# Kernel tuning notes

Hardware: AMD Instinct MI355X
Metric: run time of the kernel (lower is better)

## Reference

```python
import jax, jax.numpy as jnp
import numpy as np

G = 4        # number of grids (batch)
L = 16384    # voxels per grid (equal-length grids)
P = 512      # patch_size
H = 8        # num_heads


def setup_inputs() -> dict:
    key = jax.random.key(0)
    k1, k2, k3, k4, k5, k6 = jax.random.split(key, 6)
    N, C = G * L, 512
    feats = jax.random.normal(k1, (N, C), dtype=jnp.float32)
    curve_codes = jax.random.randint(k2, (N,), 0, 1 << 30, dtype=jnp.int64)
    Wqkv = jax.random.normal(k3, (3 * C, C), dtype=jnp.float32) * 0.02
    bqkv = jax.random.normal(k4, (3 * C,), dtype=jnp.float32) * 0.02
    Wproj = jax.random.normal(k5, (C, C), dtype=jnp.float32) * 0.02
    bproj = jax.random.normal(k6, (C,), dtype=jnp.float32) * 0.02
    return {"feats": feats, "curve_codes": curve_codes, "Wqkv": Wqkv,
            "bqkv": bqkv, "Wproj": Wproj, "bproj": bproj}


def reference(feats, curve_codes, Wqkv, bqkv, Wproj, bproj):
    N, C = feats.shape
    D = C // H
    scale = D ** -0.5
    # per-grid space-filling-curve sort -> global permutation indices
    codes = curve_codes.reshape(G, L)
    perm = (jnp.argsort(codes, axis=1) + jnp.arange(G)[:, None] * L).reshape(N)
    x = feats[perm]                                   # curve-sorted voxels
    qkv = x @ Wqkv.T + bqkv                           # [N, 3C]
    # contiguous patches of size P (grid lengths divisible by P)
    qkv = qkv.reshape(N // P, P, 3, H, D)
    q, k, v = qkv[:, :, 0], qkv[:, :, 1], qkv[:, :, 2]  # [nP, P, H, D]
    scores = jnp.einsum('nphd,nqhd->nhpq', q, k) * scale
    attn = jax.nn.softmax(scores, axis=-1)
    out = jnp.einsum('nhpq,nqhd->nphd', attn, v).reshape(N, C)
    # inverse permutation: out_final[perm[j]] = out[j]
    out = jnp.zeros_like(out).at[perm].set(out)
    return out @ Wproj.T + bproj
```

## Files before the change

kernel.cpp:

```cpp
#include <hip/hip_runtime.h>
#include <hip/hip_bf16.h>


typedef unsigned long long u64;
typedef unsigned short ushort_t;
typedef __attribute__((ext_vector_type(8))) short short8v;
typedef __attribute__((ext_vector_type(4))) float f32x4;

#define MFMA_BF16 __builtin_amdgcn_mfma_f32_16x16x32_bf16

__device__ __forceinline__ unsigned short f2bf(float f) {
  union { float f; unsigned u; } v; v.f = f;
  return (unsigned short)((v.u + 0x7FFFu + ((v.u >> 16) & 1u)) >> 16);
}

__device__ __forceinline__ unsigned pk2(float a, float b) {
  __hip_bfloat162 h = __float22bfloat162_rn(float2{a, b});
  unsigned u; __builtin_memcpy(&u, &h, 4); return u;
}

__device__ __forceinline__ void async16(ushort_t* lds, const ushort_t* g) {
  __builtin_amdgcn_global_load_lds(
      (const __attribute__((address_space(1))) unsigned int*)g,
      (__attribute__((address_space(3))) unsigned int*)lds, 16, 0, 0);
}


__global__ __launch_bounds__(512) void sort_chunk(const int* __restrict__ codes,
                                                  u64* __restrict__ keys) {
  __shared__ u64 sk[4096];
  const int base = blockIdx.x * 4096;
  for (int t = threadIdx.x; t < 4096; t += 512) {
    int e = base + t;
    sk[t] = (((u64)(unsigned)codes[e]) << 14) | (u64)(e & 16383);
  }
  __syncthreads();
  for (int k = 2; k <= 4096; k <<= 1) {
    for (int j = k >> 1; j > 0; j >>= 1) {
      for (int t = threadIdx.x; t < 4096; t += 512) {
        int jx = t ^ j;
        if (jx > t) {
          bool up = (((base + t) & 16383 & k) == 0);
          u64 a = sk[t], b = sk[jx];
          if ((a > b) == up) { sk[t] = b; sk[jx] = a; }
        }
      }
      __syncthreads();
    }
  }
  for (int t = threadIdx.x; t < 4096; t += 512) keys[base + t] = sk[t];
}

__global__ __launch_bounds__(256) void sort_gpass(u64* __restrict__ keys, int k, int j) {
  int t = blockIdx.x * 256 + threadIdx.x;
  int jx = t ^ j;
  if (jx > t) {
    bool up = ((t & 16383 & k) == 0);
    u64 a = keys[t], b = keys[jx];
    if ((a > b) == up) { keys[t] = b; keys[jx] = a; }
  }
}

__global__ __launch_bounds__(512) void sort_finish(u64* __restrict__ keys, int k) {
  __shared__ u64 sk[4096];
  const int base = blockIdx.x * 4096;
  for (int t = threadIdx.x; t < 4096; t += 512) sk[t] = keys[base + t];
  __syncthreads();
  for (int j = 2048; j > 0; j >>= 1) {
    for (int t = threadIdx.x; t < 4096; t += 512) {
      int jx = t ^ j;
      if (jx > t) {
        bool up = (((base + t) & 16383 & k) == 0);
        u64 a = sk[t], b = sk[jx];
        if ((a > b) == up) { sk[t] = b; sk[jx] = a; }
      }
    }
    __syncthreads();
  }
  for (int t = threadIdx.x; t < 4096; t += 512) keys[base + t] = sk[t];
}

__global__ __launch_bounds__(256) void write_perm(const u64* __restrict__ keys,
                                                  int* __restrict__ perm) {
  int t = blockIdx.x * 256 + threadIdx.x;
  int g = t >> 14;
  int a = (int)(keys[t] & 16383);
  perm[t] = (g << 14) | a;
}


__global__ __launch_bounds__(256) void gather_bf16(const float* __restrict__ feats,
    const int* __restrict__ perm, ushort_t* __restrict__ A) {
  int t = blockIdx.x * 256 + threadIdx.x;
  int m = t >> 5;
  int off = (t & 31) << 4;
  const float* src = feats + (size_t)perm[m] * 512 + off;
  float4 a = ((const float4*)src)[0];
  float4 b = ((const float4*)src)[1];
  float4 c = ((const float4*)src)[2];
  float4 d = ((const float4*)src)[3];
  short8v lo = { (short)f2bf(a.x), (short)f2bf(a.y), (short)f2bf(a.z), (short)f2bf(a.w),
                 (short)f2bf(b.x), (short)f2bf(b.y), (short)f2bf(b.z), (short)f2bf(b.w) };
  short8v hi = { (short)f2bf(c.x), (short)f2bf(c.y), (short)f2bf(c.z), (short)f2bf(c.w),
                 (short)f2bf(d.x), (short)f2bf(d.y), (short)f2bf(d.z), (short)f2bf(d.w) };
  ushort_t* dst = A + (size_t)m * 512 + off;
  *(short8v*)(dst) = lo;
  *(short8v*)(dst + 8) = hi;
}

__global__ __launch_bounds__(256) void convert_bf16(const float* __restrict__ src,
                                                    ushort_t* __restrict__ dst) {
  int t = blockIdx.x * 256 + threadIdx.x;
  const float* s = src + (size_t)t * 8;
  float4 a = ((const float4*)s)[0];
  float4 b = ((const float4*)s)[1];
  short8v v = { (short)f2bf(a.x), (short)f2bf(a.y), (short)f2bf(a.z), (short)f2bf(a.w),
                (short)f2bf(b.x), (short)f2bf(b.y), (short)f2bf(b.z), (short)f2bf(b.w) };
  *(short8v*)(dst + (size_t)t * 8) = v;
}


__global__ __launch_bounds__(256) void qkv_gemm(const ushort_t* __restrict__ A,
    const ushort_t* __restrict__ W, const float* __restrict__ bias,
    ushort_t* __restrict__ Q, ushort_t* __restrict__ Ko, ushort_t* __restrict__ Vt)
{
  __shared__ __align__(16) ushort_t la[128 * 64];
  __shared__ __align__(16) ushort_t lb[128 * 64];
  const int bid = blockIdx.x;
  const int swz = (bid & 7) * 768 + (bid >> 3);
  const int bx = swz % 12, by = swz / 12;
  const int rowBase = by * 128, colBase = bx * 128;
  const int tid = threadIdx.x, lane = tid & 63, w = tid >> 6;
  const int wr = w >> 1, wc = w & 1;
  const int li = lane & 15, kb = lane >> 4;
  const int lr = lane >> 3;
  const int lcs = (((lane & 7) ^ lr) << 3);
  f32x4 acc[4][4] = {};
  for (int kt = 0; kt < 8; ++kt) {
#pragma unroll
    for (int i = 0; i < 4; ++i) {
      int c = w * 4 + i;
      async16(la + c * 512, A + (size_t)(rowBase + c * 8 + lr) * 512 + kt * 64 + lcs);
      async16(lb + c * 512, W + (size_t)(colBase + c * 8 + lr) * 512 + kt * 64 + lcs);
    }
    __syncthreads();
    short8v af[2][4], bfr[2][4];
#pragma unroll
    for (int kk = 0; kk < 2; ++kk)
#pragma unroll
      for (int t = 0; t < 4; ++t) {
        int sl = ((kk * 4 + kb) ^ (li & 7)) << 3;
        af[kk][t]  = *(const short8v*)(la + (wr * 64 + t * 16 + li) * 64 + sl);
        bfr[kk][t] = *(const short8v*)(lb + (wc * 64 + t * 16 + li) * 64 + sl);
      }
#pragma unroll
    for (int kk = 0; kk < 2; ++kk)
#pragma unroll
      for (int i = 0; i < 4; ++i)
#pragma unroll
        for (int j = 0; j < 4; ++j)
          acc[i][j] = MFMA_BF16(af[kk][i], bfr[kk][j], acc[i][j], 0, 0, 0);
    __syncthreads();
  }
  const int c0 = colBase + wc * 64;
  ushort_t* tw = (w < 2) ? (la + w * 4096) : (lb + (w - 2) * 4096);
  if (c0 >= 1024) {
    char* twb = (char*)tw;
#pragma unroll
    for (int j = 0; j < 4; ++j) {
      int dloc = j * 16 + li;
      float bv = bias[c0 + dloc];
#pragma unroll
      for (int i = 0; i < 4; ++i) {
        unsigned u0 = pk2(acc[i][j][0] + bv, acc[i][j][1] + bv);
        unsigned u1 = pk2(acc[i][j][2] + bv, acc[i][j][3] + bv);
        int s = i * 2 + (kb >> 1);
        int byte = dloc * 128 + ((s ^ (dloc & 7)) << 4) + ((kb & 1) << 3);
        *(uint2*)(twb + byte) = make_uint2(u0, u1);
      }
    }
    const int h = (c0 - 1024) >> 6;
    const size_t nh = (size_t)((rowBase >> 9) * 8 + h);
    const int pbase = ((rowBase + wr * 64) & 511) + ((lane & 7) << 3);
    ushort_t* vb = Vt + nh * 32768 + pbase;
#pragma unroll
    for (int ps = 0; ps < 8; ++ps) {
      int dloc = ps * 8 + (lane >> 3);
      int byte = dloc * 128 + ((((lane & 7)) ^ (dloc & 7)) << 4);
      short8v vv = *(const short8v*)(twb + byte);
      *(short8v*)(vb + dloc * 512) = vv;
    }
  } else {
    const bool isQ = (c0 >> 9) == 0;
    const float qs = isQ ? 0.180336879f : 1.0f;
    unsigned* twd = (unsigned*)tw;
#pragma unroll
    for (int j = 0; j < 4; ++j) {
      int dl = j * 16 + li;
      float bv = bias[c0 + dl];
#pragma unroll
      for (int i = 0; i < 4; ++i)
#pragma unroll
        for (int r = 0; r < 4; ++r) {
          int p = i * 16 + kb * 4 + r;
          unsigned short hv = f2bf((acc[i][j][r] + bv) * qs);
          int dw = (dl >> 1) ^ (kb << 3);
          *((ushort_t*)(twd + p * 32 + dw) + (dl & 1)) = hv;
        }
    }
    const int hq = (c0 >> 6) & 7;
    const size_t nh = (size_t)((rowBase >> 9) * 8 + hq);
    const int p0w = (rowBase + wr * 64) & 511;
    ushort_t* qb = (isQ ? Q : Ko) + (nh * 512 + p0w) * 64 + ((lane & 7) << 3);
    const int prow = lane >> 3;
#pragma unroll
    for (int ps = 0; ps < 8; ++ps) {
      int p = ps * 8 + prow;
      int dw0 = ((lane & 7) << 2) ^ ((((p >> 2) & 3)) << 3);
      short8v vv = *(const short8v*)(twd + p * 32 + dw0);
      *(short8v*)(qb + (size_t)p * 64) = vv;
    }
  }
}


#define TILE_EXP(S, LACC, PB) do {                                             \
  _Pragma("unroll")                                                            \
  for (int t = 0; t < 4; ++t)                                                  \
    _Pragma("unroll")                                                          \
    for (int r = 0; r < 4; ++r) S[t][r] = exp2f(S[t][r]);                      \
  float q0 = (S[0][0] + S[0][1]) + (S[0][2] + S[0][3]);                        \
  float q1 = (S[1][0] + S[1][1]) + (S[1][2] + S[1][3]);                        \
  float q2 = (S[2][0] + S[2][1]) + (S[2][2] + S[2][3]);                        \
  float q3 = (S[3][0] + S[3][1]) + (S[3][2] + S[3][3]);                        \
  LACC += (q0 + q1) + (q2 + q3);                                               \
  _Pragma("unroll")                                                            \
  for (int t = 0; t < 4; ++t) {                                                \
    unsigned plo = pk2(S[t][0], S[t][1]);                                      \
    unsigned phi = pk2(S[t][2], S[t][3]);                                      \
    *(uint2*)((char*)(PB) + (((2 * t + (kb >> 1)) << 8) | (li << 4) |          \
                             ((kb & 1) << 3))) = make_uint2(plo, phi);         \
  }                                                                            \
} while (0)

__global__ __launch_bounds__(256, 2) void attn_kernel(const ushort_t* __restrict__ Q,
    const ushort_t* __restrict__ K, const ushort_t* __restrict__ Vt,
    const int* __restrict__ perm, ushort_t* __restrict__ O)
{
  __shared__ __align__(16) ushort_t kbuf[2][64][64];
  __shared__ __align__(16) ushort_t vbuf[2][64][64];
  __shared__ __align__(16) ushort_t pbuf[4][1024];
  const int b = blockIdx.x;
  const int qc = (b >> 3) & 3;
  const int nh = ((b >> 5) << 3) | (b & 7);
  const int n = nh >> 3, h = nh & 7;
  const int tid = threadIdx.x, w = tid >> 6, lane = tid & 63;
  const int li = lane & 15, kb = lane >> 4;
  const ushort_t* Qb = Q + (size_t)nh * (512 * 64);
  const ushort_t* Kb = K + (size_t)nh * (512 * 64);
  const ushort_t* Vb = Vt + (size_t)nh * (64 * 512);
  const int p0 = qc * 128 + w * 32;

  const int srow = lane >> 3;
  const int ssw = (((lane & 7) ^ srow) << 3);
  const ushort_t* Ksrc = Kb + (size_t)(w * 8 + srow) * 64 + ssw;
  const ushort_t* Vsrc = Vb + (size_t)(w * 8 + srow) * 512 + ssw;

  short8v qa0 = *(const short8v*)(Qb + (size_t)(p0 + li) * 64 + kb * 8);
  short8v qa1 = *(const short8v*)(Qb + (size_t)(p0 + li) * 64 + 32 + kb * 8);
  short8v qb0 = *(const short8v*)(Qb + (size_t)(p0 + 16 + li) * 64 + kb * 8);
  short8v qb1 = *(const short8v*)(Qb + (size_t)(p0 + 16 + li) * 64 + 32 + kb * 8);

  f32x4 oa[4] = {}, ob[4] = {};
  float la_ = 0.f, lb_ = 0.f;
  ushort_t* pb = &pbuf[w][0];
  const int sl0 = (kb ^ (li & 7)) << 3;
  const int sl1 = ((kb + 4) ^ (li & 7)) << 3;
  const char* prd0 = (const char*)pb + ((kb << 8) | (li << 4));
  const char* prd1 = (const char*)pb + (((kb + 4) << 8) | (li << 4));

  async16(&kbuf[0][w * 8][0], Ksrc);
  async16(&kbuf[0][w * 8 + 32][0], Ksrc + 2048);
  async16(&vbuf[0][w * 8][0], Vsrc);
  async16(&vbuf[0][w * 8 + 32][0], Vsrc + 16384);
  __syncthreads();

#pragma unroll 1
  for (int ch = 0; ch < 8; ++ch) {
    const int bi = ch & 1;
    if (ch < 7) {
      async16(&kbuf[bi ^ 1][w * 8][0], Ksrc + (size_t)(ch + 1) * 4096);
      async16(&kbuf[bi ^ 1][w * 8 + 32][0], Ksrc + (size_t)(ch + 1) * 4096 + 2048);
      async16(&vbuf[bi ^ 1][w * 8][0], Vsrc + (ch + 1) * 64);
      async16(&vbuf[bi ^ 1][w * 8 + 32][0], Vsrc + (ch + 1) * 64 + 16384);
    }
    f32x4 sA[4], sB[4];
#pragma unroll
    for (int t = 0; t < 4; ++t) {
      short8v kf0 = *(const short8v*)(&kbuf[bi][t * 16 + li][sl0]);
      short8v kf1 = *(const short8v*)(&kbuf[bi][t * 16 + li][sl1]);
      f32x4 zA = {0.f, 0.f, 0.f, 0.f}, zB = {0.f, 0.f, 0.f, 0.f};
      zA = MFMA_BF16(kf0, qa0, zA, 0, 0, 0);
      zB = MFMA_BF16(kf0, qb0, zB, 0, 0, 0);
      zA = MFMA_BF16(kf1, qa1, zA, 0, 0, 0);
      zB = MFMA_BF16(kf1, qb1, zB, 0, 0, 0);
      sA[t] = zA; sB[t] = zB;
    }
    short8v pa0, pa1, pb0, pb1;
    TILE_EXP(sA, la_, pb);
    pa0 = *(const short8v*)(prd0);
    pa1 = *(const short8v*)(prd1);
    TILE_EXP(sB, lb_, pb);
    pb0 = *(const short8v*)(prd0);
    pb1 = *(const short8v*)(prd1);
    __builtin_amdgcn_s_setprio(1);
#pragma unroll
    for (int dt = 0; dt < 4; ++dt) {
      short8v vf0 = *(const short8v*)(&vbuf[bi][dt * 16 + li][sl0]);
      short8v vf1 = *(const short8v*)(&vbuf[bi][dt * 16 + li][sl1]);
      oa[dt] = MFMA_BF16(pa0, vf0, oa[dt], 0, 0, 0);
      oa[dt] = MFMA_BF16(pa1, vf1, oa[dt], 0, 0, 0);
      ob[dt] = MFMA_BF16(pb0, vf0, ob[dt], 0, 0, 0);
      ob[dt] = MFMA_BF16(pb1, vf1, ob[dt], 0, 0, 0);
    }
    __builtin_amdgcn_s_setprio(0);
    __syncthreads();
    __builtin_amdgcn_sched_barrier(0);
  }
  la_ += __shfl_xor(la_, 16, 64);
  la_ += __shfl_xor(la_, 32, 64);
  lb_ += __shfl_xor(lb_, 16, 64);
  lb_ += __shfl_xor(lb_, 32, 64);
  {
    float iv = 1.0f / la_;
    float iv4[4];
#pragma unroll
    for (int r = 0; r < 4; ++r) iv4[r] = __shfl(iv, (kb << 2) + r, 16);
    int op[4];
#pragma unroll
    for (int r = 0; r < 4; ++r) op[r] = perm[n * 512 + p0 + kb * 4 + r];
#pragma unroll
    for (int dt = 0; dt < 4; ++dt)
#pragma unroll
      for (int r = 0; r < 4; ++r)
        O[(size_t)op[r] * 512 + h * 64 + dt * 16 + li] = f2bf(oa[dt][r] * iv4[r]);
  }
  {
    float iv = 1.0f / lb_;
    float iv4[4];
#pragma unroll
    for (int r = 0; r < 4; ++r) iv4[r] = __shfl(iv, (kb << 2) + r, 16);
    int op[4];
#pragma unroll
    for (int r = 0; r < 4; ++r) op[r] = perm[n * 512 + p0 + 16 + kb * 4 + r];
#pragma unroll
    for (int dt = 0; dt < 4; ++dt)
#pragma unroll
      for (int r = 0; r < 4; ++r)
        O[(size_t)op[r] * 512 + h * 64 + dt * 16 + li] = f2bf(ob[dt][r] * iv4[r]);
  }
}


__global__ __launch_bounds__(256) void proj_gemm(const ushort_t* __restrict__ A,
    const ushort_t* __restrict__ W, const float* __restrict__ bias,
    float* __restrict__ out)
{
  __shared__ __align__(16) ushort_t la[128 * 64];
  __shared__ __align__(16) ushort_t lb[128 * 64];
  const int bid = blockIdx.x;
  const int swz = (bid & 7) * 256 + (bid >> 3);
  const int bx = swz & 3, by = swz >> 2;
  const int rowBase = by * 128, colBase = bx * 128;
  const int tid = threadIdx.x, lane = tid & 63, w = tid >> 6;
  const int wr = w >> 1, wc = w & 1;
  const int li = lane & 15, kb = lane >> 4;
  const int lr = lane >> 3;
  const int lcs = (((lane & 7) ^ lr) << 3);
  f32x4 acc[4][4] = {};
  for (int kt = 0; kt < 8; ++kt) {
#pragma unroll
    for (int i = 0; i < 4; ++i) {
      int c = w * 4 + i;
      async16(la + c * 512, A + (size_t)(rowBase + c * 8 + lr) * 512 + kt * 64 + lcs);
      async16(lb + c * 512, W + (size_t)(colBase + c * 8 + lr) * 512 + kt * 64 + lcs);
    }
    __syncthreads();
    short8v af[2][4], bfr[2][4];
#pragma unroll
    for (int kk = 0; kk < 2; ++kk)
#pragma unroll
      for (int t = 0; t < 4; ++t) {
        int sl = ((kk * 4 + kb) ^ (li & 7)) << 3;
        af[kk][t]  = *(const short8v*)(la + (wr * 64 + t * 16 + li) * 64 + sl);
        bfr[kk][t] = *(const short8v*)(lb + (wc * 64 + t * 16 + li) * 64 + sl);
      }
#pragma unroll
    for (int kk = 0; kk < 2; ++kk)
#pragma unroll
      for (int i = 0; i < 4; ++i)
#pragma unroll
        for (int j = 0; j < 4; ++j)
          acc[i][j] = MFMA_BF16(af[kk][i], bfr[kk][j], acc[i][j], 0, 0, 0);
    __syncthreads();
  }
#pragma unroll
  for (int i = 0; i < 4; ++i)
#pragma unroll
    for (int j = 0; j < 4; ++j) {
      int col = colBase + wc * 64 + j * 16 + li;
      float bv = bias[col];
#pragma unroll
      for (int r = 0; r < 4; ++r) {
        int m = rowBase + wr * 64 + i * 16 + kb * 4 + r;
        out[(size_t)m * 512 + col] = acc[i][j][r] + bv;
      }
    }
}


extern "C" void kernel_launch(void* const* d_in, const int* in_sizes, int n_in,
                              void* d_out, int out_size, void* d_ws, size_t ws_size,
                              hipStream_t stream) {
  (void)in_sizes; (void)n_in; (void)out_size; (void)ws_size;
  const float* feats      = (const float*)d_in[0];
  const int* codes        = (const int*)d_in[1];
  const float* Wqkv       = (const float*)d_in[2];
  const float* bqkv       = (const float*)d_in[3];
  const float* Wproj      = (const float*)d_in[4];
  const float* bproj      = (const float*)d_in[5];
  float* out = (float*)d_out;

  char* ws = (char*)d_ws;
  int* perm = (int*)(ws);
  u64* keys = (u64*)(ws + 262144);
  ushort_t* Abf     = (ushort_t*)(ws + 1048576);
  ushort_t* att     = Abf;
  ushort_t* Wqkvbf  = (ushort_t*)(ws + 1048576 + 67108864);
  ushort_t* Wprojbf = (ushort_t*)(ws + 1048576 + 67108864 + 1572864);
  ushort_t* Qb      = (ushort_t*)(ws + 1048576 + 67108864 + 2097152);
  ushort_t* Kb      = Qb + 33554432ull;
  ushort_t* Vt      = Kb + 33554432ull;

  sort_chunk<<<16, 512, 0, stream>>>(codes, keys);
  sort_gpass<<<256, 256, 0, stream>>>(keys, 8192, 4096);
  sort_finish<<<16, 512, 0, stream>>>(keys, 8192);
  sort_gpass<<<256, 256, 0, stream>>>(keys, 16384, 8192);
  sort_gpass<<<256, 256, 0, stream>>>(keys, 16384, 4096);
  sort_finish<<<16, 512, 0, stream>>>(keys, 16384);
  write_perm<<<256, 256, 0, stream>>>(keys, perm);

  gather_bf16<<<8192, 256, 0, stream>>>(feats, perm, Abf);
  convert_bf16<<<384, 256, 0, stream>>>(Wqkv, Wqkvbf);
  convert_bf16<<<128, 256, 0, stream>>>(Wproj, Wprojbf);

  qkv_gemm<<<6144, 256, 0, stream>>>(Abf, Wqkvbf, bqkv, Qb, Kb, Vt);
  attn_kernel<<<4096, 256, 0, stream>>>(Qb, Kb, Vt, perm, att);
  proj_gemm<<<2048, 256, 0, stream>>>(att, Wprojbf, bproj, out);
}
```

Baseline: 432.5 us.

## Double query rows per attention block and fuse perm write into final sort

Each attention block now handles 256 query rows per head (64 per wave) instead of 128, so every K/V tile loaded into LDS serves twice as many queries. The grid is halved and the exp/pack step is interleaved per tile into a doubled P buffer. This raises register pressure, which could hurt occupancy under the 2-wave-per-SIMD launch bound. Separately, the last bitonic merge stage writes the permutation directly, removing the write_perm launch and one pass over the keys.

```diff
diff --git a/kernel.cpp b/kernel.cpp
--- a/kernel.cpp
+++ b/kernel.cpp
@@ -80,12 +80,25 @@
   for (int t = threadIdx.x; t < 4096; t += 512) keys[base + t] = sk[t];
 }
 
-__global__ __launch_bounds__(256) void write_perm(const u64* __restrict__ keys,
-                                                  int* __restrict__ perm) {
-  int t = blockIdx.x * 256 + threadIdx.x;
-  int g = t >> 14;
-  int a = (int)(keys[t] & 16383);
-  perm[t] = (g << 14) | a;
+__global__ __launch_bounds__(512) void sort_finish_last(const u64* __restrict__ keys,
+                                                        int* __restrict__ perm) {
+  __shared__ u64 sk[4096];
+  const int base = blockIdx.x * 4096;
+  const int g = blockIdx.x >> 2;
+  for (int t = threadIdx.x; t < 4096; t += 512) sk[t] = keys[base + t];
+  __syncthreads();
+  for (int j = 2048; j > 0; j >>= 1) {
+    for (int t = threadIdx.x; t < 4096; t += 512) {
+      int jx = t ^ j;
+      if (jx > t) {
+        u64 a = sk[t], b = sk[jx];
+        if (a > b) { sk[t] = b; sk[jx] = a; }
+      }
+    }
+    __syncthreads();
+  }
+  for (int t = threadIdx.x; t < 4096; t += 512)
+    perm[base + t] = (g << 14) | (int)(sk[t] & 16383);
 }
 
 
@@ -224,23 +237,14 @@
 }
 
 
-#define TILE_EXP(S, LACC, PB) do {                                             \
-  _Pragma("unroll")                                                            \
-  for (int t = 0; t < 4; ++t)                                                  \
-    _Pragma("unroll")                                                          \
-    for (int r = 0; r < 4; ++r) S[t][r] = exp2f(S[t][r]);                      \
-  float q0 = (S[0][0] + S[0][1]) + (S[0][2] + S[0][3]);                        \
-  float q1 = (S[1][0] + S[1][1]) + (S[1][2] + S[1][3]);                        \
-  float q2 = (S[2][0] + S[2][1]) + (S[2][2] + S[2][3]);                        \
-  float q3 = (S[3][0] + S[3][1]) + (S[3][2] + S[3][3]);                        \
-  LACC += (q0 + q1) + (q2 + q3);                                               \
-  _Pragma("unroll")                                                            \
-  for (int t = 0; t < 4; ++t) {                                                \
-    unsigned plo = pk2(S[t][0], S[t][1]);                                      \
-    unsigned phi = pk2(S[t][2], S[t][3]);                                      \
-    *(uint2*)((char*)(PB) + (((2 * t + (kb >> 1)) << 8) | (li << 4) |          \
-                             ((kb & 1) << 3))) = make_uint2(plo, phi);         \
-  }                                                                            \
+#define EXP_PACK_T(Z, LACC, PBASE, T) do {                                     \
+  Z[0] = exp2f(Z[0]); Z[1] = exp2f(Z[1]);                                      \
+  Z[2] = exp2f(Z[2]); Z[3] = exp2f(Z[3]);                                      \
+  LACC += (Z[0] + Z[1]) + (Z[2] + Z[3]);                                       \
+  unsigned plo = pk2(Z[0], Z[1]);                                              \
+  unsigned phi = pk2(Z[2], Z[3]);                                              \
+  *(uint2*)((char*)(PBASE) + (((2 * (T) + (kb >> 1)) << 8) | (li << 4) |       \
+                              ((kb & 1) << 3))) = make_uint2(plo, phi);        \
 } while (0)
 
 __global__ __launch_bounds__(256, 2) void attn_kernel(const ushort_t* __restrict__ Q,
@@ -249,17 +253,17 @@
 {
   __shared__ __align__(16) ushort_t kbuf[2][64][64];
   __shared__ __align__(16) ushort_t vbuf[2][64][64];
-  __shared__ __align__(16) ushort_t pbuf[4][1024];
+  __shared__ __align__(16) ushort_t pbuf[4][2][1024];
   const int b = blockIdx.x;
-  const int qc = (b >> 3) & 3;
-  const int nh = ((b >> 5) << 3) | (b & 7);
+  const int qc = (b >> 3) & 1;
+  const int nh = ((b >> 4) << 3) | (b & 7);
   const int n = nh >> 3, h = nh & 7;
   const int tid = threadIdx.x, w = tid >> 6, lane = tid & 63;
   const int li = lane & 15, kb = lane >> 4;
   const ushort_t* Qb = Q + (size_t)nh * (512 * 64);
   const ushort_t* Kb = K + (size_t)nh * (512 * 64);
   const ushort_t* Vb = Vt + (size_t)nh * (64 * 512);
-  const int p0 = qc * 128 + w * 32;
+  const int p0 = qc * 256 + w * 64;
 
   const int srow = lane >> 3;
   const int ssw = (((lane & 7) ^ srow) << 3);
@@ -270,14 +274,19 @@
   short8v qa1 = *(const short8v*)(Qb + (size_t)(p0 + li) * 64 + 32 + kb * 8);
   short8v qb0 = *(const short8v*)(Qb + (size_t)(p0 + 16 + li) * 64 + kb * 8);
   short8v qb1 = *(const short8v*)(Qb + (size_t)(p0 + 16 + li) * 64 + 32 + kb * 8);
-
-  f32x4 oa[4] = {}, ob[4] = {};
-  float la_ = 0.f, lb_ = 0.f;
-  ushort_t* pb = &pbuf[w][0];
+  short8v qc0 = *(const short8v*)(Qb + (size_t)(p0 + 32 + li) * 64 + kb * 8);
+  short8v qc1 = *(const short8v*)(Qb + (size_t)(p0 + 32 + li) * 64 + 32 + kb * 8);
+  short8v qd0 = *(const short8v*)(Qb + (size_t)(p0 + 48 + li) * 64 + kb * 8);
+  short8v qd1 = *(const short8v*)(Qb + (size_t)(p0 + 48 + li) * 64 + 32 + kb * 8);
+
+  f32x4 oa[4] = {}, ob[4] = {}, oc[4] = {}, od[4] = {};
+  float la_ = 0.f, lb_ = 0.f, lc_ = 0.f, ld_ = 0.f;
+  ushort_t* pbA = &pbuf[w][0][0];
+  ushort_t* pbB = &pbuf[w][1][0];
   const int sl0 = (kb ^ (li & 7)) << 3;
   const int sl1 = ((kb + 4) ^ (li & 7)) << 3;
-  const char* prd0 = (const char*)pb + ((kb << 8) | (li << 4));
-  const char* prd1 = (const char*)pb + (((kb + 4) << 8) | (li << 4));
+  const int pr0 = (kb << 8) | (li << 4);
+  const int pr1 = ((kb + 4) << 8) | (li << 4);
 
   async16(&kbuf[0][w * 8][0], Ksrc);
   async16(&kbuf[0][w * 8 + 32][0], Ksrc + 2048);
@@ -294,7 +303,7 @@
       async16(&vbuf[bi ^ 1][w * 8][0], Vsrc + (ch + 1) * 64);
       async16(&vbuf[bi ^ 1][w * 8 + 32][0], Vsrc + (ch + 1) * 64 + 16384);
     }
-    f32x4 sA[4], sB[4];
+    short8v pa0, pa1, pb0, pb1, pc0, pc1, pd0, pd1;
 #pragma unroll
     for (int t = 0; t < 4; ++t) {
       short8v kf0 = *(const short8v*)(&kbuf[bi][t * 16 + li][sl0]);
@@ -304,15 +313,29 @@
       zB = MFMA_BF16(kf0, qb0, zB, 0, 0, 0);
       zA = MFMA_BF16(kf1, qa1, zA, 0, 0, 0);
       zB = MFMA_BF16(kf1, qb1, zB, 0, 0, 0);
-      sA[t] = zA; sB[t] = zB;
-    }
-    short8v pa0, pa1, pb0, pb1;
-    TILE_EXP(sA, la_, pb);
-    pa0 = *(const short8v*)(prd0);
-    pa1 = *(const short8v*)(prd1);
-    TILE_EXP(sB, lb_, pb);
-    pb0 = *(const short8v*)(prd0);
-    pb1 = *(const short8v*)(prd1);
+      EXP_PACK_T(zA, la_, pbA, t);
+      EXP_PACK_T(zB, lb_, pbB, t);
+    }
+    pa0 = *(const short8v*)((const char*)pbA + pr0);
+    pa1 = *(const short8v*)((const char*)pbA + pr1);
+    pb0 = *(const short8v*)((const char*)pbB + pr0);
+    pb1 = *(const short8v*)((const char*)pbB + pr1);
+#pragma unroll
+    for (int t = 0; t < 4; ++t) {
+      short8v kf0 = *(const short8v*)(&kbuf[bi][t * 16 + li][sl0]);
+      short8v kf1 = *(const short8v*)(&kbuf[bi][t * 16 + li][sl1]);
+      f32x4 zC = {0.f, 0.f, 0.f, 0.f}, zD = {0.f, 0.f, 0.f, 0.f};
+      zC = MFMA_BF16(kf0, qc0, zC, 0, 0, 0);
+      zD = MFMA_BF16(kf0, qd0, zD, 0, 0, 0);
+      zC = MFMA_BF16(kf1, qc1, zC, 0, 0, 0);
+      zD = MFMA_BF16(kf1, qd1, zD, 0, 0, 0);
+      EXP_PACK_T(zC, lc_, pbA, t);
+      EXP_PACK_T(zD, ld_, pbB, t);
+    }
+    pc0 = *(const short8v*)((const char*)pbA + pr0);
+    pc1 = *(const short8v*)((const char*)pbA + pr1);
+    pd0 = *(const short8v*)((const char*)pbB + pr0);
+    pd1 = *(const short8v*)((const char*)pbB + pr1);
     __builtin_amdgcn_s_setprio(1);
 #pragma unroll
     for (int dt = 0; dt < 4; ++dt) {
@@ -322,43 +345,38 @@
       oa[dt] = MFMA_BF16(pa1, vf1, oa[dt], 0, 0, 0);
       ob[dt] = MFMA_BF16(pb0, vf0, ob[dt], 0, 0, 0);
       ob[dt] = MFMA_BF16(pb1, vf1, ob[dt], 0, 0, 0);
+      oc[dt] = MFMA_BF16(pc0, vf0, oc[dt], 0, 0, 0);
+      oc[dt] = MFMA_BF16(pc1, vf1, oc[dt], 0, 0, 0);
+      od[dt] = MFMA_BF16(pd0, vf0, od[dt], 0, 0, 0);
+      od[dt] = MFMA_BF16(pd1, vf1, od[dt], 0, 0, 0);
     }
     __builtin_amdgcn_s_setprio(0);
     __syncthreads();
     __builtin_amdgcn_sched_barrier(0);
   }
-  la_ += __shfl_xor(la_, 16, 64);
-  la_ += __shfl_xor(la_, 32, 64);
-  lb_ += __shfl_xor(lb_, 16, 64);
-  lb_ += __shfl_xor(lb_, 32, 64);
-  {
-    float iv = 1.0f / la_;
-    float iv4[4];
-#pragma unroll
-    for (int r = 0; r < 4; ++r) iv4[r] = __shfl(iv, (kb << 2) + r, 16);
-    int op[4];
-#pragma unroll
-    for (int r = 0; r < 4; ++r) op[r] = perm[n * 512 + p0 + kb * 4 + r];
-#pragma unroll
-    for (int dt = 0; dt < 4; ++dt)
-#pragma unroll
-      for (int r = 0; r < 4; ++r)
-        O[(size_t)op[r] * 512 + h * 64 + dt * 16 + li] = f2bf(oa[dt][r] * iv4[r]);
-  }
-  {
-    float iv = 1.0f / lb_;
-    float iv4[4];
-#pragma unroll
-    for (int r = 0; r < 4; ++r) iv4[r] = __shfl(iv, (kb << 2) + r, 16);
-    int op[4];
-#pragma unroll
-    for (int r = 0; r < 4; ++r) op[r] = perm[n * 512 + p0 + 16 + kb * 4 + r];
-#pragma unroll
-    for (int dt = 0; dt < 4; ++dt)
-#pragma unroll
-      for (int r = 0; r < 4; ++r)
-        O[(size_t)op[r] * 512 + h * 64 + dt * 16 + li] = f2bf(ob[dt][r] * iv4[r]);
-  }
+#define EPI(OACC, L, POFF) do {                                                \
+    float l2 = (L) + __shfl_xor((L), 16, 64);                                  \
+    l2 += __shfl_xor(l2, 32, 64);                                              \
+    float iv = 1.0f / l2;                                                      \
+    float iv4[4];                                                              \
+    _Pragma("unroll")                                                          \
+    for (int r = 0; r < 4; ++r) iv4[r] = __shfl(iv, (kb << 2) + r, 16);        \
+    int op[4];                                                                 \
+    _Pragma("unroll")                                                          \
+    for (int r = 0; r < 4; ++r)                                                \
+      op[r] = perm[n * 512 + p0 + (POFF) + kb * 4 + r];                        \
+    _Pragma("unroll")                                                          \
+    for (int dt = 0; dt < 4; ++dt)                                             \
+      _Pragma("unroll")                                                        \
+      for (int r = 0; r < 4; ++r)                                              \
+        O[(size_t)op[r] * 512 + h * 64 + dt * 16 + li] =                       \
+            f2bf(OACC[dt][r] * iv4[r]);                                        \
+  } while (0)
+  EPI(oa, la_, 0);
+  EPI(ob, lb_, 16);
+  EPI(oc, lc_, 32);
+  EPI(od, ld_, 48);
+#undef EPI
 }
 
 
@@ -447,14 +465,13 @@
   sort_finish<<<16, 512, 0, stream>>>(keys, 8192);
   sort_gpass<<<256, 256, 0, stream>>>(keys, 16384, 8192);
   sort_gpass<<<256, 256, 0, stream>>>(keys, 16384, 4096);
-  sort_finish<<<16, 512, 0, stream>>>(keys, 16384);
-  write_perm<<<256, 256, 0, stream>>>(keys, perm);
+  sort_finish_last<<<16, 512, 0, stream>>>(keys, perm);
 
   gather_bf16<<<8192, 256, 0, stream>>>(feats, perm, Abf);
   convert_bf16<<<384, 256, 0, stream>>>(Wqkv, Wqkvbf);
   convert_bf16<<<128, 256, 0, stream>>>(Wproj, Wprojbf);
 
   qkv_gemm<<<6144, 256, 0, stream>>>(Abf, Wqkvbf, bqkv, Qb, Kb, Vt);
-  attn_kernel<<<4096, 256, 0, stream>>>(Qb, Kb, Vt, perm, att);
+  attn_kernel<<<2048, 256, 0, stream>>>(Qb, Kb, Vt, perm, att);
   proj_gemm<<<2048, 256, 0, stream>>>(att, Wprojbf, bproj, out);
 }
```

Measured after the change: 448.4 us. 1.04x slower.
